# Kernel optimization log

Hardware: AMD Instinct MI355X
Metric: run time of the kernel (lower is better)

Reference implementation:

```python
import jax, jax.numpy as jnp
import numpy as np

B, L, C = 8, 256, 64
NEG = -1e30  # large negative instead of -inf to keep grads NaN-free


def setup_inputs() -> dict:
    key = jax.random.key(0)
    k1, k2 = jax.random.split(key)
    scores = jax.random.normal(k1, (B, L, L, C), dtype=jnp.float32)
    lens = jax.random.randint(k2, (B,), 64, L, dtype=jnp.int32)  # sentence lengths in [64, L-1]
    return {"scores": scores, "lens": lens}


def _inside_max(scores, lens):
    """Max-semiring CKY inside pass. scores: [B,L,L,C]; returns logZ per batch [B]."""
    t = jnp.transpose(jnp.max(scores, axis=-1), (1, 2, 0))  # [L,L,B] best label per span
    s0 = jnp.zeros((L, L, B), scores.dtype)                 # chart s[i,j] = best score of span (i,j)
    i = jnp.arange(L)
    j = jnp.arange(L)

    def step(s, w):
        e = jnp.clip(i + w, 0, L - 1)                       # span end, [L]
        k = jnp.clip(i[:, None] + j[None, :], 0, L - 1)     # split points, [L,L]
        left = s[i[:, None], k]                             # s[i, i+j], [L,L,B]
        right = s[k, e[:, None]]                            # s[i+j, i+w], [L,L,B]
        valid = (j[None, :] >= 1) & (j[None, :] < w) & ((i + w) < L)[:, None]
        comb = jnp.max(jnp.where(valid[..., None], left + right, NEG), axis=1)  # [L,B]
        s_l = t[i, e]                                       # label-max span score, [L,B]
        diag = jnp.where(w == 1, s_l, comb + s_l)
        row_ok = ((i + w) < L)[:, None]
        upd = jnp.where(row_ok, diag, s[i, e])
        s = s.at[i, e].set(upd)
        return s, None

    s, _ = jax.lax.scan(step, s0, jnp.arange(1, L))
    lens_c = jnp.clip(lens, 1, L - 1)
    return s[0, lens_c, jnp.arange(B)]                      # logZ (best tree score) per sentence


def reference(scores, lens):
    return _inside_max(scores, lens)
```

## Files before the change

### kernel.cpp

```cpp
#include <hip/hip_runtime.h>

#define LVAL 256
#define T    32
#define ST   36
#define SLAB (T * ST)
#define NB   8
#define NEG  (-1e30f)

typedef float f32x4 __attribute__((ext_vector_type(4)));

#define SOFT_FENCE() asm volatile("" ::: "memory")

__device__ __forceinline__ size_t sidx(int b, int i, int e) {
    return ((size_t)b << 16) + (i << 8) + e;
}

__device__ __forceinline__ void st_coh4(float* p, f32x4 v) {
    asm volatile("global_store_dwordx4 %0, %1, off sc0 sc1"
                 :: "v"(p), "v"(v) : "memory");
}
__device__ __forceinline__ f32x4 ld_coh4(const float* p) {
    f32x4 v;
    asm volatile("global_load_dwordx4 %0, %1, off sc0 sc1\n\t"
                 "s_waitcnt vmcnt(0)"
                 : "=&v"(v) : "v"(p) : "memory");
    return v;
}
__device__ __forceinline__ void ld_coh4x4(const float* p,
                                          f32x4& a, f32x4& b, f32x4& c, f32x4& d) {
    asm volatile("global_load_dwordx4 %0, %4, off sc0 sc1\n\t"
                 "global_load_dwordx4 %1, %4, off offset:16 sc0 sc1\n\t"
                 "global_load_dwordx4 %2, %4, off offset:32 sc0 sc1\n\t"
                 "global_load_dwordx4 %3, %4, off offset:48 sc0 sc1\n\t"
                 "s_waitcnt vmcnt(0)"
                 : "=&v"(a), "=&v"(b), "=&v"(c), "=&v"(d)
                 : "v"(p) : "memory");
}

template<int CTRL>
__device__ __forceinline__ float dpp_max(float v) {
#if __has_builtin(__builtin_amdgcn_mov_dpp)
    int o = __builtin_amdgcn_mov_dpp(__builtin_bit_cast(int, v), CTRL, 0xF, 0xF, true);
    return fmaxf(v, __builtin_bit_cast(float, o));
#else
    return fmaxf(v, __shfl_xor(v, CTRL == 0xB1 ? 1 : 2));
#endif
}

__device__ __forceinline__ int opaque_zero(float x) {
    int z;
    asm("v_and_b32 %0, 0, %1" : "=v"(z) : "v"(__float_as_int(x)));
    return z;
}

__device__ __forceinline__ float red8(const f32x4 a, const f32x4 b,
                                      const f32x4 c, const f32x4 d) {
    float m0 = fmaxf(a.x + b.x, a.y + b.y);
    float m1 = fmaxf(a.z + b.z, a.w + b.w);
    float m2 = fmaxf(c.x + d.x, c.y + d.y);
    float m3 = fmaxf(c.z + d.z, c.w + d.w);
    return fmaxf(fmaxf(m0, m1), fmaxf(m2, m3));
}
__device__ __forceinline__ float red4(const f32x4 a, const f32x4 b) {
    float m0 = fmaxf(a.x + b.x, a.y + b.y);
    float m1 = fmaxf(a.z + b.z, a.w + b.w);
    return fmaxf(m0, m1);
}

__global__ __launch_bounds__(256) void phase1(const float* __restrict__ scores,
                                              float* __restrict__ s,
                                              int* __restrict__ bar) {
    if (blockIdx.x == 0 && blockIdx.y == 0) {
        for (int k = threadIdx.x; k < 2048; k += 256) bar[k] = 0;
    }
    const int i = blockIdx.x, b = blockIdx.y;
    const int sub = threadIdx.x & 15, slot = threadIdx.x >> 4;
    const float* row = scores + ((((size_t)b * LVAL + i) * LVAL) << 6);
    #pragma unroll 4
    for (int m0 = 0; m0 < LVAL; m0 += 16) {
        const int e = m0 + slot;
        if (e > i) {
            float4 v = *((const float4*)(row + ((size_t)e << 6)) + sub);
            float mx = fmaxf(fmaxf(v.x, v.y), fmaxf(v.z, v.w));
            #pragma unroll
            for (int d = 1; d < 16; d <<= 1) mx = fmaxf(mx, __shfl_xor(mx, d));
            if (sub == 0) s[sidx(b, i, e)] = mx;
        }
    }
}

struct EC {
    f32x4 a[4], ct[4], cu[4], bt[4];
    float tv, pr, afr, bfr;
};

__device__ __forceinline__ EC eprefetch(int l, int c, int p, int z,
        const float (*Ae)[ST], const float (*BeT)[ST],
        const float (*cur)[ST], const float (*curT)[ST],
        const float (*tb)[ST], const float (*pre)[ST]) {
    EC e;
    const int delta = l - (T - 1);
    const int ad = delta < 0 ? -delta : delta;
    const int cells = T - ad;
    const bool g = c < cells;
    int li = g ? (delta < 0 ? c + ad : c) : 0;
    int le = g ? li + delta : 0;
    li += z; le += z;
    e.tv  = tb[li][le];
    e.pr  = pre[li][le];
    e.afr = Ae[li][li + 1];
    e.bfr = BeT[le][le > 0 ? le - 1 : 0];
    #pragma unroll
    for (int m = 0; m < 4; ++m) {
        const int k0 = 4 * (p + 2 * m);
        e.a[m]  = *(const f32x4*)&Ae[li][k0];
        e.ct[m] = *(const f32x4*)&curT[le][k0];
        e.cu[m] = *(const f32x4*)&cur[li][k0];
        e.bt[m] = *(const f32x4*)&BeT[le][k0];
    }
    return e;
}

__device__ __forceinline__ float ecompute(int l, int c, int p, int D,
        const EC& e, float vprev, float vn,
        float (*cur)[ST], float (*curT)[ST]) {
    const int delta = l - (T - 1);
    const int ad = delta < 0 ? -delta : delta;
    const int cells = T - ad;
    const bool g = c < cells;
    const int li = g ? (delta < 0 ? c + ad : c) : 0;
    const int le = g ? li + delta : 0;
    const bool dpos = delta > 0;
    float acc = e.pr;
    #pragma unroll
    for (int m = 0; m < 4; ++m)
        acc = fmaxf(acc, red8(e.a[m], e.ct[m], e.cu[m], e.bt[m]));
    const float srcL = dpos ? vn : vprev;
    const float srcR = dpos ? vprev : vn;
    const bool okL = dpos || (c != cells - 1);
    const bool okR = dpos || (c != 0);
    acc = fmaxf(acc, okL ? e.afr + srcL : NEG);
    acc = fmaxf(acc, okR ? srcR + e.bfr : NEG);
    acc = dpp_max<0xB1>(acc);
    const float v = (D == 1 && l == 0) ? e.tv : acc + e.tv;
    if (g && p == 0) cur[li][le] = v;
    if (g && p == 1) curT[le][li] = v;
    return g ? v : NEG;
}

struct EC0 { f32x4 cu[4], ct[4]; float tvs, tfr; };

__device__ __forceinline__ EC0 e0prefetch(int l, int c, int p, int z,
        const float (*cur0)[ST], const float (*curT0)[ST], const float (*t0)[ST]) {
    EC0 e;
    const int cells = T - l;
    const bool g = c < cells;
    int li = c;
    int le = g ? c + l : c;
    li += z; le += z;
    e.tvs = t0[li][le];
    e.tfr = t0[le - 1][le];
    #pragma unroll
    for (int m = 0; m < 4; ++m) {
        const int k0 = 4 * (p + 2 * m);
        e.cu[m] = *(const f32x4*)&cur0[li][k0];
        e.ct[m] = *(const f32x4*)&curT0[le][k0];
    }
    return e;
}

__device__ __forceinline__ float e0compute(int l, int c, int p,
        const EC0& e, float vprev, float vn, float t0d,
        float (*cur0)[ST], float (*curT0)[ST]) {
    const int cells = T - l;
    const bool g = c < cells;
    const int li = c;
    const int le = g ? c + l : c;
    float acc = fmaxf(t0d + vn, vprev + e.tfr);
    #pragma unroll
    for (int m = 0; m < 4; ++m)
        acc = fmaxf(acc, red4(e.cu[m], e.ct[m]));
    acc = dpp_max<0xB1>(acc);
    const float v = acc + e.tvs;
    if (g && p == 0) cur0[li][le] = v;
    if (g && p == 1) curT0[le][li] = v;
    return g ? v : NEG;
}

__device__ __forceinline__ void batch_barrier(int* __restrict__ bar, int b,
                                              int tid, int ep) {
    asm volatile("s_waitcnt vmcnt(0)" ::: "memory");
    __syncthreads();
    if (tid == 0) {
        int* cnt  = bar + b * 256;
        int* flag = bar + b * 256 + 64;
        int prev = __hip_atomic_fetch_add(cnt, 1, __ATOMIC_RELAXED,
                                          __HIP_MEMORY_SCOPE_AGENT);
        if ((prev & (NB - 1)) == NB - 1) {
            __hip_atomic_store(flag, ep, __ATOMIC_RELAXED, __HIP_MEMORY_SCOPE_AGENT);
        } else {
            int guard = 0;
            while (__hip_atomic_load(flag, __ATOMIC_RELAXED,
                                     __HIP_MEMORY_SCOPE_AGENT) < ep) {
                __builtin_amdgcn_s_sleep(2);
                if (++guard > (1 << 22)) break;
            }
        }
    }
    __syncthreads();
}

__global__ __launch_bounds__(256) void dp_fused(float* __restrict__ s,
                                                const int* __restrict__ lens,
                                                float* __restrict__ out,
                                                int* __restrict__ bar) {
    __shared__ __align__(16) float smem[14 * SLAB];
    float* ATb = smem;
    float (*Ae)[ST]  = (float(*)[ST])(smem + 6 * SLAB);
    float (*tb)[ST]  = (float(*)[ST])(smem + 7 * SLAB);
    float (*BeT)[ST] = (float(*)[ST])(smem + 8 * SLAB);
    float (*cur)[ST] = (float(*)[ST])(smem + 9 * SLAB);
    float* BWb = smem + 10 * SLAB;
    float (*pre)[ST] = (float(*)[ST])BWb;

    const int b  = blockIdx.x & 7;
    const int bi = blockIdx.x >> 3;
    const int tid = threadIdx.x, wid = tid >> 6, lane = tid & 63;
    const int lr = tid >> 5, lc = tid & 31;
    const int grow = lane >> 1, gc = (lane & 1) * 16;
    const int gly = lane >> 3, glx = lane & 7, r0 = 4 * gly, c0 = 4 * glx;
    const int trow = tid >> 3, tc4 = (tid & 7) * 4;
    float (*BW)[ST] = (float(*)[ST])(BWb + wid * SLAB);
    const int c = lane >> 1, p = lane & 1;

    if (wid == 0) {
        float (*curT0)[ST] = (float(*)[ST])(BWb + 1 * SLAB);
        float (*t0)[ST]    = (float(*)[ST])(BWb + 2 * SLAB);
        const float4 negv = make_float4(NEG, NEG, NEG, NEG);
        #pragma unroll
        for (int j = 0; j < 4; ++j) {
            float4 v = *(const float4*)&s[sidx(b, bi * T + grow, bi * T + gc + 4 * j)];
            *(float4*)&t0[grow][gc + 4 * j]    = v;
            *(float4*)&Ae[grow][gc + 4 * j]    = negv;
            *(float4*)&curT0[grow][gc + 4 * j] = negv;
        }
        SOFT_FENCE();
        if (lane < T - 1) {
            float v = t0[lane][lane + 1];
            Ae[lane][lane + 1] = v;
            curT0[lane + 1][lane] = v;
        }
        SOFT_FENCE();
        const float t0d = t0[c][c + 1];
        float vprev = t0d;
        EC0 fA = e0prefetch(2, c, p, 0, Ae, curT0, t0);
        EC0 fB;
        #pragma unroll 1
        for (int l = 2; l < T; l += 2) {
            {
                float vn = __shfl(vprev, lane + 2);
                int z = opaque_zero(vn);
                fB = e0prefetch(l + 1, c, p, z, Ae, curT0, t0);
                vprev = e0compute(l, c, p, fA, vprev, vn, t0d, Ae, curT0);
                SOFT_FENCE();
            }
            {
                float vn = __shfl(vprev, lane + 2);
                int z = opaque_zero(vn);
                if (l + 2 < T) fA = e0prefetch(l + 2, c, p, z, Ae, curT0, t0);
                vprev = e0compute(l + 1, c, p, fB, vprev, vn, t0d, Ae, curT0);
                SOFT_FENCE();
            }
        }
        #pragma unroll
        for (int j = 0; j < 4; ++j)
            st_coh4(&s[sidx(b, bi * T + grow, bi * T + gc + 4 * j)],
                    *(const f32x4*)&Ae[grow][gc + 4 * j]);
    } else if (bi + 1 < NB) {
        for (int idx = tid - 64; idx < 256; idx += 192) {
            const int row = idx >> 3, c4 = (idx & 7) * 4;
            *(float4*)&tb[row][c4] =
                *(const float4*)&s[sidx(b, bi * T + row, (bi + 1) * T + c4)];
        }
    }

    #pragma unroll 1
    for (int D = 1; D < NB; ++D) {
        batch_barrier(bar, b, tid, D);
        const int be = bi + D;
        if (be < NB) {
            if (D == 1) {
                f32x4 v = ld_coh4(&s[sidx(b, be * T + trow, be * T + tc4)]);
                BeT[tc4 + 0][trow] = (trow < tc4 + 0) ? v[0] : NEG;
                BeT[tc4 + 1][trow] = (trow < tc4 + 1) ? v[1] : NEG;
                BeT[tc4 + 2][trow] = (trow < tc4 + 2) ? v[2] : NEG;
                BeT[tc4 + 3][trow] = (trow < tc4 + 3) ? v[3] : NEG;
            }
            const int nw = (D - 1 < 4) ? (D - 1) : 4;
            float ag[4][4];
            #pragma unroll
            for (int i = 0; i < 4; ++i)
                #pragma unroll
                for (int j = 0; j < 4; ++j) ag[i][j] = NEG;
            for (int K = bi + 1 + wid; K < be; K += 4) {
                const float (*AT)[ST] = (const float(*)[ST])(ATb + (K - bi - 1) * SLAB);
                f32x4 b0, b1, b2, b3;
                ld_coh4x4(&s[sidx(b, K * T + grow, be * T + gc)], b0, b1, b2, b3);
                *(f32x4*)&BW[grow][gc + 0]  = b0;
                *(f32x4*)&BW[grow][gc + 4]  = b1;
                *(f32x4*)&BW[grow][gc + 8]  = b2;
                *(f32x4*)&BW[grow][gc + 12] = b3;
                SOFT_FENCE();
                #pragma unroll 4
                for (int k = 0; k < T; ++k) {
                    float4 a4 = *(const float4*)&AT[k][r0];
                    float4 b4 = *(const float4*)&BW[k][c0];
                    const float aa[4] = {a4.x, a4.y, a4.z, a4.w};
                    const float bb[4] = {b4.x, b4.y, b4.z, b4.w};
                    #pragma unroll
                    for (int i = 0; i < 4; ++i)
                        #pragma unroll
                        for (int j = 0; j < 4; ++j)
                            ag[i][j] = fmaxf(ag[i][j], aa[i] + bb[j]);
                }
                SOFT_FENCE();
            }
            if (wid < nw) {
                #pragma unroll
                for (int i = 0; i < 4; ++i)
                    *(float4*)&BW[r0 + i][c0] =
                        make_float4(ag[i][0], ag[i][1], ag[i][2], ag[i][3]);
            }
            __syncthreads();
            #pragma unroll
            for (int r = 0; r < 4; ++r) {
                const int row = lr + 8 * r;
                float v = NEG;
                for (int w2 = 0; w2 < nw; ++w2)
                    v = fmaxf(v, BWb[w2 * SLAB + row * ST + lc]);
                pre[row][lc] = v;
            }
            __syncthreads();
            float (*curT)[ST] = (D == NB - 1) ? (float(*)[ST])(BWb + 1 * SLAB)
                                              : (float(*)[ST])(ATb + (D - 1) * SLAB);
            #pragma unroll
            for (int r = 0; r < 4; ++r) {
                const int row = lr + 8 * r;
                cur[row][lc]  = NEG;
                curT[row][lc] = NEG;
            }
            __syncthreads();
            if (wid == 0) {
                EC eA = eprefetch(0, c, p, 0, Ae, BeT, cur, curT, tb, pre);
                EC eB;
                float vprev = NEG;
                #pragma unroll 1
                for (int l = 0; l < 2 * T; l += 2) {
                    {
                        const bool dpos = (l > T - 1);
                        float vn = __shfl(vprev, lane + (dpos ? 2 : -2));
                        int z = opaque_zero(vn);
                        eB = eprefetch(l + 1, c, p, z, Ae, BeT, cur, curT, tb, pre);
                        vprev = ecompute(l, c, p, D, eA, vprev, vn, cur, curT);
                        SOFT_FENCE();
                    }
                    {
                        const bool dpos = (l + 1 > T - 1);
                        float vn = __shfl(vprev, lane + (dpos ? 2 : -2));
                        int z = opaque_zero(vn);
                        if (l + 2 < 2 * T)
                            eA = eprefetch(l + 2, c, p, z, Ae, BeT, cur, curT, tb, pre);
                        vprev = ecompute(l + 1, c, p, D, eB, vprev, vn, cur, curT);
                        SOFT_FENCE();
                    }
                }
            }
            __syncthreads();
            {
                f32x4 pv = *(const f32x4*)&cur[trow][tc4];
                st_coh4(&s[sidx(b, bi * T + trow, be * T + tc4)], pv);
            }
            if (be + 1 < NB) {
                *(float4*)&tb[trow][tc4] =
                    *(const float4*)&s[sidx(b, bi * T + trow, (be + 1) * T + tc4)];
                f32x4 v = ld_coh4(&s[sidx(b, (be + 1) * T + trow,
                                          (be + 1) * T + tc4)]);
                BeT[tc4 + 0][trow] = (trow < tc4 + 0) ? v[0] : NEG;
                BeT[tc4 + 1][trow] = (trow < tc4 + 1) ? v[1] : NEG;
                BeT[tc4 + 2][trow] = (trow < tc4 + 2) ? v[2] : NEG;
                BeT[tc4 + 3][trow] = (trow < tc4 + 3) ? v[3] : NEG;
            }
        }
    }

    if (bi == 0 && tid == 0) {
        int len = lens[b];
        len = len < 1 ? 1 : (len > LVAL - 1 ? LVAL - 1 : len);
        const int K = len >> 5, off = len & 31;
        float r;
        if (K == 0)           r = Ae[0][off];
        else if (K == NB - 1) r = cur[0][off];
        else                  r = ATb[(K - 1) * SLAB + off * ST];
        out[b] = r;
    }
}

extern "C" void kernel_launch(void* const* d_in, const int* in_sizes, int n_in,
                              void* d_out, int out_size, void* d_ws, size_t ws_size,
                              hipStream_t stream) {
    const float* scores = (const float*)d_in[0];
    const int*   lens   = (const int*)d_in[1];
    float*       out    = (float*)d_out;
    float*       s      = (float*)d_ws;
    int*         bar    = (int*)((char*)d_ws + ((size_t)(8) << 16) * sizeof(float));

    phase1<<<dim3(LVAL, 8), 256, 0, stream>>>(scores, s, bar);
    dp_fused<<<64, 256, 0, stream>>>(s, lens, out, bar);
}
```

Baseline: 359.8 us.

## Prefetch next diagonal's B blocks into registers while wave 0 runs the chain

```diff
diff --git a/kernel.cpp b/kernel.cpp
--- a/kernel.cpp
+++ b/kernel.cpp
@@ -45,12 +45,6 @@
 #else
     return fmaxf(v, __shfl_xor(v, CTRL == 0xB1 ? 1 : 2));
 #endif
-}
-
-__device__ __forceinline__ int opaque_zero(float x) {
-    int z;
-    asm("v_and_b32 %0, 0, %1" : "=v"(z) : "v"(__float_as_int(x)));
-    return z;
 }
 
 __device__ __forceinline__ float red8(const f32x4 a, const f32x4 b,
@@ -94,7 +88,7 @@
     float tv, pr, afr, bfr;
 };
 
-__device__ __forceinline__ EC eprefetch(int l, int c, int p, int z,
+__device__ __forceinline__ EC eprefetch(int l, int c, int p,
         const float (*Ae)[ST], const float (*BeT)[ST],
         const float (*cur)[ST], const float (*curT)[ST],
         const float (*tb)[ST], const float (*pre)[ST]) {
@@ -103,9 +97,8 @@
     const int ad = delta < 0 ? -delta : delta;
     const int cells = T - ad;
     const bool g = c < cells;
-    int li = g ? (delta < 0 ? c + ad : c) : 0;
-    int le = g ? li + delta : 0;
-    li += z; le += z;
+    const int li = g ? (delta < 0 ? c + ad : c) : 0;
+    const int le = g ? li + delta : 0;
     e.tv  = tb[li][le];
     e.pr  = pre[li][le];
     e.afr = Ae[li][li + 1];
@@ -150,14 +143,13 @@
 
 struct EC0 { f32x4 cu[4], ct[4]; float tvs, tfr; };
 
-__device__ __forceinline__ EC0 e0prefetch(int l, int c, int p, int z,
+__device__ __forceinline__ EC0 e0prefetch(int l, int c, int p,
         const float (*cur0)[ST], const float (*curT0)[ST], const float (*t0)[ST]) {
     EC0 e;
     const int cells = T - l;
     const bool g = c < cells;
-    int li = c;
-    int le = g ? c + l : c;
-    li += z; le += z;
+    const int li = c;
+    const int le = g ? c + l : c;
     e.tvs = t0[li][le];
     e.tfr = t0[le - 1][le];
     #pragma unroll
@@ -185,6 +177,21 @@
     if (g && p == 0) cur0[li][le] = v;
     if (g && p == 1) curT0[le][li] = v;
     return g ? v : NEG;
+}
+
+__device__ __forceinline__ void gemm_blk(const float* ATs, const float (*BW)[ST],
+                                         int r0, int c0, float (&ag)[4][4]) {
+    const float (*AT)[ST] = (const float(*)[ST])ATs;
+    #pragma unroll 4
+    for (int k = 0; k < T; ++k) {
+        f32x4 a4 = *(const f32x4*)&AT[k][r0];
+        f32x4 b4 = *(const f32x4*)&BW[k][c0];
+        #pragma unroll
+        for (int i = 0; i < 4; ++i)
+            #pragma unroll
+            for (int j = 0; j < 4; ++j)
+                ag[i][j] = fmaxf(ag[i][j], a4[i] + b4[j]);
+    }
 }
 
 __device__ __forceinline__ void batch_barrier(int* __restrict__ bar, int b,
@@ -233,6 +240,9 @@
     float (*BW)[ST] = (float(*)[ST])(BWb + wid * SLAB);
     const int c = lane >> 1, p = lane & 1;
 
+    f32x4 pbA[4], pbB[4];
+    f32x4 tpb[4], bpb[4];
+
     if (wid == 0) {
         float (*curT0)[ST] = (float(*)[ST])(BWb + 1 * SLAB);
         float (*t0)[ST]    = (float(*)[ST])(BWb + 2 * SLAB);
@@ -253,21 +263,22 @@
         SOFT_FENCE();
         const float t0d = t0[c][c + 1];
         float vprev = t0d;
-        EC0 fA = e0prefetch(2, c, p, 0, Ae, curT0, t0);
+        SOFT_FENCE();
+        EC0 fA = e0prefetch(2, c, p, Ae, curT0, t0);
         EC0 fB;
         #pragma unroll 1
         for (int l = 2; l < T; l += 2) {
             {
                 float vn = __shfl(vprev, lane + 2);
-                int z = opaque_zero(vn);
-                fB = e0prefetch(l + 1, c, p, z, Ae, curT0, t0);
+                asm volatile("" :: "v"(vn) : "memory");
+                fB = e0prefetch(l + 1, c, p, Ae, curT0, t0);
                 vprev = e0compute(l, c, p, fA, vprev, vn, t0d, Ae, curT0);
                 SOFT_FENCE();
             }
             {
                 float vn = __shfl(vprev, lane + 2);
-                int z = opaque_zero(vn);
-                if (l + 2 < T) fA = e0prefetch(l + 2, c, p, z, Ae, curT0, t0);
+                asm volatile("" :: "v"(vn) : "memory");
+                if (l + 2 < T) fA = e0prefetch(l + 2, c, p, Ae, curT0, t0);
                 vprev = e0compute(l + 1, c, p, fB, vprev, vn, t0d, Ae, curT0);
                 SOFT_FENCE();
             }
@@ -302,28 +313,34 @@
             for (int i = 0; i < 4; ++i)
                 #pragma unroll
                 for (int j = 0; j < 4; ++j) ag[i][j] = NEG;
-            for (int K = bi + 1 + wid; K < be; K += 4) {
-                const float (*AT)[ST] = (const float(*)[ST])(ATb + (K - bi - 1) * SLAB);
-                f32x4 b0, b1, b2, b3;
-                ld_coh4x4(&s[sidx(b, K * T + grow, be * T + gc)], b0, b1, b2, b3);
-                *(f32x4*)&BW[grow][gc + 0]  = b0;
-                *(f32x4*)&BW[grow][gc + 4]  = b1;
-                *(f32x4*)&BW[grow][gc + 8]  = b2;
-                *(f32x4*)&BW[grow][gc + 12] = b3;
-                SOFT_FENCE();
-                #pragma unroll 4
-                for (int k = 0; k < T; ++k) {
-                    float4 a4 = *(const float4*)&AT[k][r0];
-                    float4 b4 = *(const float4*)&BW[k][c0];
-                    const float aa[4] = {a4.x, a4.y, a4.z, a4.w};
-                    const float bb[4] = {b4.x, b4.y, b4.z, b4.w};
-                    #pragma unroll
-                    for (int i = 0; i < 4; ++i)
+            if (D >= 2) {
+                if (wid == 0) {
+                    f32x4 b0, b1, b2, b3;
+                    ld_coh4x4(&s[sidx(b, (bi + 1) * T + grow, be * T + gc)],
+                              b0, b1, b2, b3);
+                    *(f32x4*)&BW[grow][gc + 0]  = b0;
+                    *(f32x4*)&BW[grow][gc + 4]  = b1;
+                    *(f32x4*)&BW[grow][gc + 8]  = b2;
+                    *(f32x4*)&BW[grow][gc + 12] = b3;
+                    SOFT_FENCE();
+                    gemm_blk(ATb + 0, BW, r0, c0, ag);
+                } else {
+                    if (wid <= D - 2) {
                         #pragma unroll
                         for (int j = 0; j < 4; ++j)
-                            ag[i][j] = fmaxf(ag[i][j], aa[i] + bb[j]);
-                }
-                SOFT_FENCE();
+                            *(f32x4*)&BW[grow][gc + 4 * j] = pbA[j];
+                        SOFT_FENCE();
+                        gemm_blk(ATb + wid * SLAB, BW, r0, c0, ag);
+                        SOFT_FENCE();
+                    }
+                    if (wid + 3 <= D - 2) {
+                        #pragma unroll
+                        for (int j = 0; j < 4; ++j)
+                            *(f32x4*)&BW[grow][gc + 4 * j] = pbB[j];
+                        SOFT_FENCE();
+                        gemm_blk(ATb + (wid + 3) * SLAB, BW, r0, c0, ag);
+                    }
+                }
             }
             if (wid < nw) {
                 #pragma unroll
@@ -351,7 +368,7 @@
             }
             __syncthreads();
             if (wid == 0) {
-                EC eA = eprefetch(0, c, p, 0, Ae, BeT, cur, curT, tb, pre);
+                EC eA = eprefetch(0, c, p, Ae, BeT, cur, curT, tb, pre);
                 EC eB;
                 float vprev = NEG;
                 #pragma unroll 1
@@ -359,20 +376,39 @@
                     {
                         const bool dpos = (l > T - 1);
                         float vn = __shfl(vprev, lane + (dpos ? 2 : -2));
-                        int z = opaque_zero(vn);
-                        eB = eprefetch(l + 1, c, p, z, Ae, BeT, cur, curT, tb, pre);
+                        asm volatile("" :: "v"(vn) : "memory");
+                        eB = eprefetch(l + 1, c, p, Ae, BeT, cur, curT, tb, pre);
                         vprev = ecompute(l, c, p, D, eA, vprev, vn, cur, curT);
                         SOFT_FENCE();
                     }
                     {
                         const bool dpos = (l + 1 > T - 1);
                         float vn = __shfl(vprev, lane + (dpos ? 2 : -2));
-                        int z = opaque_zero(vn);
+                        asm volatile("" :: "v"(vn) : "memory");
                         if (l + 2 < 2 * T)
-                            eA = eprefetch(l + 2, c, p, z, Ae, BeT, cur, curT, tb, pre);
+                            eA = eprefetch(l + 2, c, p, Ae, BeT, cur, curT, tb, pre);
                         vprev = ecompute(l + 1, c, p, D, eB, vprev, vn, cur, curT);
                         SOFT_FENCE();
                     }
+                }
+            } else if (be + 1 < NB) {
+                if (wid <= D - 1)
+                    ld_coh4x4(&s[sidx(b, (bi + 1 + wid) * T + grow, (be + 1) * T + gc)],
+                              pbA[0], pbA[1], pbA[2], pbA[3]);
+                if (wid + 3 <= D - 1)
+                    ld_coh4x4(&s[sidx(b, (bi + 4 + wid) * T + grow, (be + 1) * T + gc)],
+                              pbB[0], pbB[1], pbB[2], pbB[3]);
+                if (wid == 1) {
+                    #pragma unroll
+                    for (int j = 0; j < 4; ++j)
+                        tpb[j] = *(const f32x4*)&s[sidx(b, bi * T + grow,
+                                                        (be + 1) * T + gc + 4 * j)];
+                }
+                if (wid == 2) {
+                    #pragma unroll
+                    for (int j = 0; j < 4; ++j)
+                        bpb[j] = ld_coh4(&s[sidx(b, (be + 1) * T + grow,
+                                                 (be + 1) * T + gc + 4 * j)]);
                 }
             }
             __syncthreads();
@@ -381,14 +417,20 @@
                 st_coh4(&s[sidx(b, bi * T + trow, be * T + tc4)], pv);
             }
             if (be + 1 < NB) {
-                *(float4*)&tb[trow][tc4] =
-                    *(const float4*)&s[sidx(b, bi * T + trow, (be + 1) * T + tc4)];
-                f32x4 v = ld_coh4(&s[sidx(b, (be + 1) * T + trow,
-                                          (be + 1) * T + tc4)]);
-                BeT[tc4 + 0][trow] = (trow < tc4 + 0) ? v[0] : NEG;
-                BeT[tc4 + 1][trow] = (trow < tc4 + 1) ? v[1] : NEG;
-                BeT[tc4 + 2][trow] = (trow < tc4 + 2) ? v[2] : NEG;
-                BeT[tc4 + 3][trow] = (trow < tc4 + 3) ? v[3] : NEG;
+                if (wid == 1) {
+                    #pragma unroll
+                    for (int j = 0; j < 4; ++j)
+                        *(f32x4*)&tb[grow][gc + 4 * j] = tpb[j];
+                }
+                if (wid == 2) {
+                    #pragma unroll
+                    for (int j = 0; j < 4; ++j)
+                        #pragma unroll
+                        for (int k = 0; k < 4; ++k) {
+                            const int col = gc + 4 * j + k;
+                            BeT[col][grow] = (grow < col) ? bpb[j][k] : NEG;
+                        }
+                }
             }
         }
     }
```

New measurement: 356.2 us. Within noise of the previous version (-1.0%).
